# Kernel tuning notes

Hardware: AMD Instinct MI355X
Metric: run time of the kernel (lower is better)

## Reference

```python
import jax, jax.numpy as jnp
import numpy as np

D_MODEL = 1024
SEQ_LEN = 32768


def setup_inputs() -> dict:
    key = jax.random.key(0)
    k1, k2, k3 = jax.random.split(key, 3)
    inputs = jax.random.normal(k1, (SEQ_LEN,), dtype=jnp.float32)
    W = jax.random.normal(k2, (D_MODEL, D_MODEL), dtype=jnp.float32) * (1.0 / np.sqrt(D_MODEL))
    b = jax.random.normal(k3, (D_MODEL,), dtype=jnp.float32) * 0.01
    return {"inputs": inputs, "W": W, "b": b}


def reference(inputs, W, b):
    d_model = W.shape[0]
    # t: [D], p: [L] -- log(1 + position)
    t = jnp.linspace(0.0, 1.0, d_model, dtype=inputs.dtype)
    p = jnp.log1p(jnp.arange(inputs.shape[0], dtype=inputs.dtype))
    # phase[l, d] = 2*pi * inputs[l] * (t[d] + p[l]); sum sin over positions
    phase = 2.0 * jnp.pi * inputs[:, None] * (t[None, :] + p[:, None])  # [L, D]
    signal = jnp.sum(jnp.sin(phase), axis=0)  # [D]
    # nn.Linear: x @ W.T + b
    return signal @ W.T + b
```

## Files before the change

### kernel.cpp

```cpp
#include <hip/hip_runtime.h>

#define L_TOTAL 32768
#define D_MODEL 1024
#define NCH     128
#define LCH     (L_TOTAL / NCH)
#define NBLK_S  (NCH * 8)

__global__ __launch_bounds__(256) void signal_kernel(const float* __restrict__ x,
                                                     float* __restrict__ part) {
    __shared__ float2 sxp[LCH];
    __shared__ float  hred[256];
    const int tid = threadIdx.x;
    const int c   = blockIdx.x >> 3;
    const int q   = blockIdx.x & 7;

    {
        const int l = c * LCH + tid;
        const float xv = x[l];
        sxp[tid] = make_float2(xv, xv * __logf(1.0f + (float)l));
    }
    __syncthreads();

    const int   dl = tid & 127;
    const int   h  = tid >> 7;
    const float t  = (float)(q * 128 + dl) * (1.0f / 1023.0f);

    float a0 = 0.f, a1 = 0.f, a2 = 0.f, a3 = 0.f;
    #pragma unroll 4
    for (int j = 0; j < 128; j += 4) {
        const float2 v0 = sxp[h * 128 + j + 0];
        const float2 v1 = sxp[h * 128 + j + 1];
        const float2 v2 = sxp[h * 128 + j + 2];
        const float2 v3 = sxp[h * 128 + j + 3];
        a0 += __builtin_amdgcn_sinf(__builtin_amdgcn_fractf(fmaf(v0.x, t, v0.y)));
        a1 += __builtin_amdgcn_sinf(__builtin_amdgcn_fractf(fmaf(v1.x, t, v1.y)));
        a2 += __builtin_amdgcn_sinf(__builtin_amdgcn_fractf(fmaf(v2.x, t, v2.y)));
        a3 += __builtin_amdgcn_sinf(__builtin_amdgcn_fractf(fmaf(v3.x, t, v3.y)));
    }
    hred[tid] = (a0 + a1) + (a2 + a3);
    __syncthreads();
    if (tid < 128)
        part[c * D_MODEL + q * 128 + tid] = hred[tid] + hred[128 + tid];
}

__global__ __launch_bounds__(1024) void finish_kernel(const float* __restrict__ W,
                                                      const float* __restrict__ b,
                                                      const float* __restrict__ part,
                                                      float* __restrict__ out) {
    __shared__ float4 red[4][256];
    __shared__ float4 ssig[256];
    __shared__ float  rsum[16];

    const int tid = threadIdx.x;
    const int blk = blockIdx.x;

    {
        const int dq = tid & 255;
        const int cs = tid >> 8;
        const float4* p4 = (const float4*)part;
        float4 A = make_float4(0.f, 0.f, 0.f, 0.f);
        float4 B = make_float4(0.f, 0.f, 0.f, 0.f);
        #pragma unroll
        for (int j = 0; j < 32; j += 2) {
            const float4 u = p4[(cs * 32 + j) * 256 + dq];
            const float4 v = p4[(cs * 32 + j + 1) * 256 + dq];
            A.x += u.x; A.y += u.y; A.z += u.z; A.w += u.w;
            B.x += v.x; B.y += v.y; B.z += v.z; B.w += v.w;
        }
        A.x += B.x; A.y += B.y; A.z += B.z; A.w += B.w;
        red[cs][dq] = A;
    }
    __syncthreads();
    if (tid < 256) {
        const float4 r0 = red[0][tid], r1 = red[1][tid];
        const float4 r2 = red[2][tid], r3 = red[3][tid];
        ssig[tid] = make_float4((r0.x + r1.x) + (r2.x + r3.x),
                                (r0.y + r1.y) + (r2.y + r3.y),
                                (r0.z + r1.z) + (r2.z + r3.z),
                                (r0.w + r1.w) + (r2.w + r3.w));
    }
    __syncthreads();

    const int  wv   = tid >> 6;
    const int  lane = tid & 63;
    const int  h    = wv & 1;
    const int  row  = blk * 8 + (wv >> 1);
    const float4* Wr = (const float4*)(W + (size_t)row * D_MODEL);
    float sum = 0.f;
    #pragma unroll
    for (int k = 0; k < 2; ++k) {
        const int idx = h * 128 + k * 64 + lane;
        const float4 w4 = Wr[idx];
        const float4 s4 = ssig[idx];
        sum += w4.x * s4.x + w4.y * s4.y + w4.z * s4.z + w4.w * s4.w;
    }
    #pragma unroll
    for (int off = 32; off > 0; off >>= 1)
        sum += __shfl_down(sum, off, 64);
    if (lane == 0) rsum[wv] = sum;
    __syncthreads();
    if (tid < 8)
        out[blk * 8 + tid] = (rsum[tid * 2] + rsum[tid * 2 + 1]) + b[blk * 8 + tid];
}

extern "C" void kernel_launch(void* const* d_in, const int* in_sizes, int n_in,
                              void* d_out, int out_size, void* d_ws, size_t ws_size,
                              hipStream_t stream) {
    const float* x = (const float*)d_in[0];
    const float* W = (const float*)d_in[1];
    const float* b = (const float*)d_in[2];
    float* out    = (float*)d_out;
    float* part   = (float*)d_ws;

    signal_kernel<<<NBLK_S, 256, 0, stream>>>(x, part);
    finish_kernel<<<D_MODEL / 8, 1024, 0, stream>>>(W, b, part, out);
}
```

Measured before the change: 70.92 us.

## Register-tile four d-columns per thread and halve position chunk count

Each thread now computes four d-columns for one shared-memory position load, cutting LDS reads per sin evaluation by four. Chunks double in length (64 chunks of 512 positions), so half as many blocks are launched and the partial buffer the finish kernel must reduce is halved. The in-block reduction now sums 8 partials per column instead of 2. The grid shrinks to 512 blocks, which lowers parallelism and may hurt occupancy on a GPU with many CUs.

```diff
diff --git a/kernel.cpp b/kernel.cpp
--- a/kernel.cpp
+++ b/kernel.cpp
@@ -2,45 +2,55 @@
 
 #define L_TOTAL 32768
 #define D_MODEL 1024
-#define NCH     128
+#define NCH     64
 #define LCH     (L_TOTAL / NCH)
 #define NBLK_S  (NCH * 8)
 
 __global__ __launch_bounds__(256) void signal_kernel(const float* __restrict__ x,
                                                      float* __restrict__ part) {
     __shared__ float2 sxp[LCH];
-    __shared__ float  hred[256];
+    __shared__ float  hred[8][128];
     const int tid = threadIdx.x;
     const int c   = blockIdx.x >> 3;
-    const int q   = blockIdx.x & 7;
+    const int dq  = blockIdx.x & 7;
 
-    {
-        const int l = c * LCH + tid;
+    #pragma unroll
+    for (int s = 0; s < 2; ++s) {
+        const int idx = tid + s * 256;
+        const int l   = c * LCH + idx;
         const float xv = x[l];
-        sxp[tid] = make_float2(xv, xv * __logf(1.0f + (float)l));
+        sxp[idx] = make_float2(xv, xv * __logf(1.0f + (float)l));
     }
     __syncthreads();
 
-    const int   dl = tid & 127;
-    const int   h  = tid >> 7;
-    const float t  = (float)(q * 128 + dl) * (1.0f / 1023.0f);
+    const int dl = tid & 31;
+    const int lh = tid >> 5;
+    const int d0 = dq * 128 + dl;
+    const float t0 = (float)(d0)       * (1.0f / 1023.0f);
+    const float t1 = (float)(d0 + 32)  * (1.0f / 1023.0f);
+    const float t2 = (float)(d0 + 64)  * (1.0f / 1023.0f);
+    const float t3 = (float)(d0 + 96)  * (1.0f / 1023.0f);
 
     float a0 = 0.f, a1 = 0.f, a2 = 0.f, a3 = 0.f;
     #pragma unroll 4
-    for (int j = 0; j < 128; j += 4) {
-        const float2 v0 = sxp[h * 128 + j + 0];
-        const float2 v1 = sxp[h * 128 + j + 1];
-        const float2 v2 = sxp[h * 128 + j + 2];
-        const float2 v3 = sxp[h * 128 + j + 3];
-        a0 += __builtin_amdgcn_sinf(__builtin_amdgcn_fractf(fmaf(v0.x, t, v0.y)));
-        a1 += __builtin_amdgcn_sinf(__builtin_amdgcn_fractf(fmaf(v1.x, t, v1.y)));
-        a2 += __builtin_amdgcn_sinf(__builtin_amdgcn_fractf(fmaf(v2.x, t, v2.y)));
-        a3 += __builtin_amdgcn_sinf(__builtin_amdgcn_fractf(fmaf(v3.x, t, v3.y)));
+    for (int j = 0; j < 64; ++j) {
+        const float2 v = sxp[lh * 64 + j];
+        a0 += __builtin_amdgcn_sinf(__builtin_amdgcn_fractf(fmaf(v.x, t0, v.y)));
+        a1 += __builtin_amdgcn_sinf(__builtin_amdgcn_fractf(fmaf(v.x, t1, v.y)));
+        a2 += __builtin_amdgcn_sinf(__builtin_amdgcn_fractf(fmaf(v.x, t2, v.y)));
+        a3 += __builtin_amdgcn_sinf(__builtin_amdgcn_fractf(fmaf(v.x, t3, v.y)));
     }
-    hred[tid] = (a0 + a1) + (a2 + a3);
+    hred[lh][dl]      = a0;
+    hred[lh][dl + 32] = a1;
+    hred[lh][dl + 64] = a2;
+    hred[lh][dl + 96] = a3;
     __syncthreads();
-    if (tid < 128)
-        part[c * D_MODEL + q * 128 + tid] = hred[tid] + hred[128 + tid];
+    if (tid < 128) {
+        float s = 0.f;
+        #pragma unroll
+        for (int l2 = 0; l2 < 8; ++l2) s += hred[l2][tid];
+        part[c * D_MODEL + dq * 128 + tid] = s;
+    }
 }
 
 __global__ __launch_bounds__(1024) void finish_kernel(const float* __restrict__ W,
@@ -61,9 +71,9 @@
         float4 A = make_float4(0.f, 0.f, 0.f, 0.f);
         float4 B = make_float4(0.f, 0.f, 0.f, 0.f);
         #pragma unroll
-        for (int j = 0; j < 32; j += 2) {
-            const float4 u = p4[(cs * 32 + j) * 256 + dq];
-            const float4 v = p4[(cs * 32 + j + 1) * 256 + dq];
+        for (int j = 0; j < 16; j += 2) {
+            const float4 u = p4[(cs * 16 + j) * 256 + dq];
+            const float4 v = p4[(cs * 16 + j + 1) * 256 + dq];
             A.x += u.x; A.y += u.y; A.z += u.z; A.w += u.w;
             B.x += v.x; B.y += v.y; B.z += v.z; B.w += v.w;
         }
```

After: 68.46 us. 3.5% less time.
